# Kernel tuning notes

Hardware: AMD Instinct MI355X
Metric: run time of the kernel (lower is better)

The kernel has to match this reference:

```python
import jax, jax.numpy as jnp
import numpy as np
import jax.ops

N_NODES = 50000
N_EDGES = 800000
N_GRAPHS = 512
F_IN = 128
HID = 256
N_CLASSES = 1

def _xavier(key, shape):
    fan_in, fan_out = shape[0], shape[1]
    std = (2.0 / (fan_in + fan_out)) ** 0.5
    return jax.random.normal(key, shape, dtype=jnp.float32) * std

def setup_inputs() -> dict:
    key = jax.random.key(0)
    ks = jax.random.split(key, 12)
    x = jax.random.normal(ks[0], (N_NODES, F_IN), dtype=jnp.float32)
    edge_index = jax.random.randint(ks[1], (2, N_EDGES), 0, N_NODES, dtype=jnp.int64)
    batch = jnp.sort(jax.random.randint(ks[2], (N_NODES,), 0, N_GRAPHS, dtype=jnp.int64))
    return {
        'x': x, 'edge_index': edge_index, 'batch': batch,
        'W0': _xavier(ks[3], (F_IN, HID)), 'b0': jnp.zeros((HID,), jnp.float32),
        'W1': _xavier(ks[4], (HID, HID)), 'b1': jnp.zeros((HID,), jnp.float32),
        'W2': _xavier(ks[5], (HID, HID)), 'b2': jnp.zeros((HID,), jnp.float32),
        'Wm1': _xavier(ks[6], (HID, HID)), 'bm1': jnp.zeros((HID,), jnp.float32),
        'Wm2': _xavier(ks[7], (HID, N_CLASSES)), 'bm2': jnp.zeros((N_CLASSES,), jnp.float32),
    }

def _gcn_layer(h, W, b, src, dst, deg_inv_sqrt):
    # PyG GCNConv: linear -> symmetric-normalized aggregation (with self loops) -> bias
    hw = h @ W                                        # [N, out]
    norm = deg_inv_sqrt[src] * deg_inv_sqrt[dst]      # [E]
    msg = hw[src] * norm[:, None]                     # [E, out]
    agg = jax.ops.segment_sum(msg, dst, num_segments=N_NODES)
    agg = agg + hw * (deg_inv_sqrt ** 2)[:, None]     # self-loop term
    return agg + b

def reference(x, edge_index, batch, W0, b0, W1, b1, W2, b2, Wm1, bm1, Wm2, bm2):
    src, dst = edge_index[0], edge_index[1]
    # degree with added self loops (in-degree at dst)
    deg = jax.ops.segment_sum(jnp.ones((N_EDGES,), jnp.float32), dst, num_segments=N_NODES) + 1.0
    deg_inv_sqrt = jax.lax.rsqrt(deg)
    h = jax.nn.relu(_gcn_layer(x, W0, b0, src, dst, deg_inv_sqrt))
    h = jax.nn.relu(_gcn_layer(h, W1, b1, src, dst, deg_inv_sqrt))
    h = jax.nn.relu(_gcn_layer(h, W2, b2, src, dst, deg_inv_sqrt))
    # global mean pool over graphs
    sums = jax.ops.segment_sum(h, batch, num_segments=N_GRAPHS)
    cnts = jax.ops.segment_sum(jnp.ones((N_NODES,), jnp.float32), batch, num_segments=N_GRAPHS)
    pooled = sums / jnp.maximum(cnts, 1.0)[:, None]   # [G, HID]
    out = jax.nn.relu(pooled @ Wm1 + bm1) @ Wm2 + bm2 # [G, num_classes]
    return out
```

## Files before the change

kernel.cpp:

```cpp
#include <hip/hip_runtime.h>

constexpr int N_NODES  = 50000;
constexpr int N_EDGES  = 800000;
constexpr int N_GRAPHS = 512;
constexpr int F_IN     = 128;
constexpr int HID      = 256;
constexpr int NPAD     = 50048;

typedef short short8 __attribute__((ext_vector_type(8)));
typedef float f32x4  __attribute__((ext_vector_type(4)));

__device__ __forceinline__ unsigned short f2b(float f) {
    unsigned u = __float_as_uint(f);
    u += 0x7fffu + ((u >> 16) & 1u);
    return (unsigned short)(u >> 16);
}
__device__ __forceinline__ float b2f_lo(unsigned u) { return __uint_as_float(u << 16); }
__device__ __forceinline__ float b2f_hi(unsigned u) { return __uint_as_float(u & 0xffff0000u); }

__global__ __launch_bounds__(256) void prep_kernel(
    const int* __restrict__ dst, int* __restrict__ deg,
    const float* __restrict__ W0, const float* __restrict__ W1, const float* __restrict__ W2,
    unsigned short* __restrict__ Wt0, unsigned short* __restrict__ Wt1, unsigned short* __restrict__ Wt2)
{
    const int b = blockIdx.x, t = threadIdx.x;
    if (b < 3125) {
        int e = b * 256 + t;
        atomicAdd(&deg[dst[e]], 1);
    } else {
        int i = (b - 3125) * 256 + t;
        const float* W; unsigned short* Wt; int K; int j;
        if (i < 32768)      { W = W0; Wt = Wt0; K = 128; j = i; }
        else if (i < 98304) { W = W1; Wt = Wt1; K = 256; j = i - 32768; }
        else                { W = W2; Wt = Wt2; K = 256; j = i - 98304; }
        int k = j >> 8, n = j & 255;
        int idx = (n >> 7) * (K * 128) + (((k >> 3) * 128 + (n & 127)) << 3) + (k & 7);
        Wt[idx] = f2b(W[j]);
    }
}

__global__ void block_sum_dis_kernel(const int* __restrict__ deg, int* __restrict__ bsum,
                                     float* __restrict__ dis, int* __restrict__ bcnt, int n) {
    __shared__ int sm[256];
    __shared__ int hist[64];
    int t = threadIdx.x, base = blockIdx.x * 1024;
    if (t < 64) hist[t] = 0;
    __syncthreads();
    int s = 0;
    #pragma unroll
    for (int i = 0; i < 4; ++i) {
        int idx = base + t + i * 256;
        if (idx < n) {
            int d = deg[idx]; s += d;
            dis[idx] = rsqrtf((float)d + 1.0f);
            atomicAdd(&hist[63 - min(d, 63)], 1);
        }
    }
    sm[t] = s; __syncthreads();
    for (int o = 128; o > 0; o >>= 1) { if (t < o) sm[t] += sm[t + o]; __syncthreads(); }
    if (t == 0) bsum[blockIdx.x] = sm[0];
    if (t < 64 && hist[t]) atomicAdd(&bcnt[t], hist[t]);
}

__global__ void scan_bsum_kernel(int* __restrict__ bsum, int nb,
                                 const int* __restrict__ bcnt, int* __restrict__ bcur) {
    __shared__ int sm[64], sb[64];
    int t = threadIdx.x;
    int v = (t < nb) ? bsum[t] : 0;
    int c = bcnt[t];
    sm[t] = v; sb[t] = c; __syncthreads();
    for (int o = 1; o < 64; o <<= 1) {
        int a = (t >= o) ? sm[t - o] : 0;
        int bb = (t >= o) ? sb[t - o] : 0;
        __syncthreads();
        sm[t] += a; sb[t] += bb;
        __syncthreads();
    }
    if (t < nb) bsum[t] = sm[t] - v;
    bcur[t] = sb[t] - c;
}

__global__ void scan_local_kernel(const int* __restrict__ deg, const int* __restrict__ bsum,
                                  int* __restrict__ cursor, int* __restrict__ bcur,
                                  int4* __restrict__ perm4, int* __restrict__ idx_of,
                                  const float* __restrict__ dis, int n) {
    __shared__ int sm[256];
    __shared__ int lcnt[64], lbase[64];
    int t = threadIdx.x, base = blockIdx.x * 1024;
    if (t < 64) lcnt[t] = 0;
    int idx0 = base + t * 4;
    int v[4], s = 0;
    #pragma unroll
    for (int i = 0; i < 4; ++i) { int id = idx0 + i; v[i] = (id < n) ? deg[id] : 0; s += v[i]; }
    sm[t] = s; __syncthreads();
    for (int o = 1; o < 256; o <<= 1) {
        int a = (t >= o) ? sm[t - o] : 0; __syncthreads();
        sm[t] += a; __syncthreads();
    }
    int excl = bsum[blockIdx.x] + sm[t] - s;
    int st[4], lp[4];
    #pragma unroll
    for (int i = 0; i < 4; ++i) {
        int id = idx0 + i;
        st[i] = excl;
        if (id < n) {
            cursor[id] = excl;
            lp[i] = atomicAdd(&lcnt[63 - min(v[i], 63)], 1);
        }
        excl += v[i];
    }
    __syncthreads();
    if (t < 64) lbase[t] = lcnt[t] ? atomicAdd(&bcur[t], lcnt[t]) : 0;
    __syncthreads();
    #pragma unroll
    for (int i = 0; i < 4; ++i) {
        int id = idx0 + i;
        if (id < n) {
            int hb = 63 - min(v[i], 63);
            int pos = lbase[hb] + lp[i];
            perm4[pos] = make_int4(id, st[i], st[i] + v[i], __float_as_int(dis[id]));
            idx_of[id] = pos;
        }
    }
}

__global__ void fill_csr(const int* __restrict__ src, const int* __restrict__ dst,
                         const float* __restrict__ dis, const int* __restrict__ idx_of,
                         int* __restrict__ cursor, int2* __restrict__ csr) {
    int e = blockIdx.x * blockDim.x + threadIdx.x;
    if (e >= N_EDGES) return;
    int s = src[e], d = dst[e];
    int pos = atomicAdd(&cursor[d], 1);
    float w = dis[s] * dis[d];
    csr[pos] = make_int2(idx_of[s], __float_as_int(w));
}

__global__ __launch_bounds__(256) void xconv_kernel(
    const float* __restrict__ x, const int4* __restrict__ perm4,
    unsigned short* __restrict__ x_bf)
{
    int t = threadIdx.x;
    int idx = blockIdx.x * 64 + (t >> 2);
    if (idx >= N_NODES) return;
    int node = perm4[idx].x;
    int c = t & 3;
    const float4* xs = reinterpret_cast<const float4*>(x + (size_t)node * 128 + c * 32);
    unsigned short* dp = x_bf + (size_t)idx * 128 + c * 32;
    #pragma unroll
    for (int u = 0; u < 8; ++u) {
        float4 v = xs[u];
        unsigned r0 = (unsigned)f2b(v.x) | ((unsigned)f2b(v.y) << 16);
        unsigned r1 = (unsigned)f2b(v.z) | ((unsigned)f2b(v.w) << 16);
        *reinterpret_cast<uint2*>(dp + u * 4) = make_uint2(r0, r1);
    }
}

template<int F>
__global__ __launch_bounds__(256) void agg_full(
    const unsigned short* __restrict__ hin, const int4* __restrict__ perm4,
    const int2* __restrict__ csr, uint4* __restrict__ out4)
{
    constexpr int LPR  = F / 8;
    constexpr int NSUB = 64 / LPR;
    constexpr int EPS  = 16 / NSUB;
    const int lane = threadIdx.x & 63;
    const int sub  = lane / LPR;
    const int fc   = lane % LPR;
    const int idx  = blockIdx.x * 4 + (threadIdx.x >> 6);
    if (idx >= N_NODES) return;
    const int4 p = perm4[idx];
    const float dn = __int_as_float(p.w);

    float acc[8];
    {
        float sw = (sub == 0) ? dn * dn : 0.0f;
        uint2 u2[2];
        *reinterpret_cast<uint4*>(u2) =
            *reinterpret_cast<const uint4*>(hin + (size_t)idx * F + fc * 8);
        #pragma unroll
        for (int h = 0; h < 2; ++h) {
            acc[h * 4 + 0] = b2f_lo(u2[h].x) * sw;
            acc[h * 4 + 1] = b2f_hi(u2[h].x) * sw;
            acc[h * 4 + 2] = b2f_lo(u2[h].y) * sw;
            acc[h * 4 + 3] = b2f_hi(u2[h].y) * sw;
        }
    }

    int j = p.y;
    const int end = p.z;

    for (; j + 16 <= end; j += 16) {
        int2 c[EPS];
        uint2 g[EPS][2];
        #pragma unroll
        for (int u = 0; u < EPS; ++u) c[u] = csr[j + sub * EPS + u];
        #pragma unroll
        for (int u = 0; u < EPS; ++u)
            *reinterpret_cast<uint4*>(g[u]) =
                *reinterpret_cast<const uint4*>(hin + (size_t)c[u].x * F + fc * 8);
        #pragma unroll
        for (int u = 0; u < EPS; ++u) {
            float w = __int_as_float(c[u].y);
            #pragma unroll
            for (int h = 0; h < 2; ++h) {
                acc[h * 4 + 0] = fmaf(b2f_lo(g[u][h].x), w, acc[h * 4 + 0]);
                acc[h * 4 + 1] = fmaf(b2f_hi(g[u][h].x), w, acc[h * 4 + 1]);
                acc[h * 4 + 2] = fmaf(b2f_lo(g[u][h].y), w, acc[h * 4 + 2]);
                acc[h * 4 + 3] = fmaf(b2f_hi(g[u][h].y), w, acc[h * 4 + 3]);
            }
        }
    }
    int jj = j + sub;
    for (; jj + NSUB < end; jj += 2 * NSUB) {
        int2 c0 = csr[jj], c1 = csr[jj + NSUB];
        uint2 g0[2], g1[2];
        *reinterpret_cast<uint4*>(g0) =
            *reinterpret_cast<const uint4*>(hin + (size_t)c0.x * F + fc * 8);
        *reinterpret_cast<uint4*>(g1) =
            *reinterpret_cast<const uint4*>(hin + (size_t)c1.x * F + fc * 8);
        float w0 = __int_as_float(c0.y), w1 = __int_as_float(c1.y);
        #pragma unroll
        for (int h = 0; h < 2; ++h) {
            acc[h * 4 + 0] = fmaf(b2f_lo(g0[h].x), w0, fmaf(b2f_lo(g1[h].x), w1, acc[h * 4 + 0]));
            acc[h * 4 + 1] = fmaf(b2f_hi(g0[h].x), w0, fmaf(b2f_hi(g1[h].x), w1, acc[h * 4 + 1]));
            acc[h * 4 + 2] = fmaf(b2f_lo(g0[h].y), w0, fmaf(b2f_lo(g1[h].y), w1, acc[h * 4 + 2]));
            acc[h * 4 + 3] = fmaf(b2f_hi(g0[h].y), w0, fmaf(b2f_hi(g1[h].y), w1, acc[h * 4 + 3]));
        }
    }
    if (jj < end) {
        int2 c0 = csr[jj];
        float w = __int_as_float(c0.y);
        uint2 g[2];
        *reinterpret_cast<uint4*>(g) =
            *reinterpret_cast<const uint4*>(hin + (size_t)c0.x * F + fc * 8);
        #pragma unroll
        for (int h = 0; h < 2; ++h) {
            acc[h * 4 + 0] = fmaf(b2f_lo(g[h].x), w, acc[h * 4 + 0]);
            acc[h * 4 + 1] = fmaf(b2f_hi(g[h].x), w, acc[h * 4 + 1]);
            acc[h * 4 + 2] = fmaf(b2f_lo(g[h].y), w, acc[h * 4 + 2]);
            acc[h * 4 + 3] = fmaf(b2f_hi(g[h].y), w, acc[h * 4 + 3]);
        }
    }

    #pragma unroll
    for (int k = 0; k < 8; ++k) {
        #pragma unroll
        for (int off = LPR; off < 64; off <<= 1)
            acc[k] += __shfl_xor(acc[k], off, 64);
    }

    if (sub == 0) {
        uint2 r[2];
        #pragma unroll
        for (int h = 0; h < 2; ++h) {
            r[h].x = (unsigned)f2b(acc[h * 4 + 0]) | ((unsigned)f2b(acc[h * 4 + 1]) << 16);
            r[h].y = (unsigned)f2b(acc[h * 4 + 2]) | ((unsigned)f2b(acc[h * 4 + 3]) << 16);
        }
        int chunk = (idx >> 7) * (128 * (F / 8)) + fc * 128 + (idx & 127);
        out4[chunk] = *reinterpret_cast<uint4*>(r);
    }
}

template<int K>
__global__ __launch_bounds__(256) void gemm_frag(
    const uint4* __restrict__ A4,
    const unsigned short* __restrict__ Wt_frag,
    const float* __restrict__ bias,
    unsigned short* __restrict__ C,
    int relu)
{
    __shared__ __align__(16) unsigned short Bs[K * 128];
    const int t    = threadIdx.x;
    const int lane = t & 63;
    const int w    = t >> 6;
    const int wm   = w & 1, wn = w >> 1;
    const int q    = lane >> 4, m = lane & 15;
    const int panel = blockIdx.x;
    const int col0  = blockIdx.y * 128;

    {
        const uint4* src4 = reinterpret_cast<const uint4*>(Wt_frag + blockIdx.y * (K * 128));
        uint4* dst4 = reinterpret_cast<uint4*>(Bs);
        #pragma unroll
        for (int it = 0; it < K / 16; ++it)
            dst4[it * 256 + t] = src4[it * 256 + t];
    }
    __syncthreads();

    f32x4 acc[4][4] = {};
    const int abase = panel * (128 * (K / 8));

    #pragma unroll
    for (int kb = 0; kb < K / 32; ++kb) {
        short8 af[4], bf[4];
        #pragma unroll
        for (int i = 0; i < 4; ++i) {
            uint4 v = A4[abase + (kb * 4 + q) * 128 + wm * 64 + i * 16 + m];
            af[i] = *reinterpret_cast<short8*>(&v);
        }
        #pragma unroll
        for (int jn = 0; jn < 4; ++jn)
            bf[jn] = *reinterpret_cast<const short8*>(&Bs[((kb * 4 + q) * 128 + wn * 64 + jn * 16 + m) * 8]);
        #pragma unroll
        for (int i = 0; i < 4; ++i)
            #pragma unroll
            for (int jn = 0; jn < 4; ++jn)
                acc[i][jn] = __builtin_amdgcn_mfma_f32_16x16x32_bf16(af[i], bf[jn], acc[i][jn], 0, 0, 0);
    }

    #pragma unroll
    for (int jn = 0; jn < 4; ++jn) {
        int col = col0 + wn * 64 + jn * 16 + m;
        float bj = bias[col];
        #pragma unroll
        for (int i = 0; i < 4; ++i) {
            int rowb = panel * 128 + wm * 64 + i * 16 + q * 4;
            #pragma unroll
            for (int r = 0; r < 4; ++r) {
                float v = acc[i][jn][r] + bj;
                if (relu) v = fmaxf(v, 0.f);
                C[(size_t)(rowb + r) * 256 + col] = f2b(v);
            }
        }
    }
}

__global__ __launch_bounds__(256) void pool_mlp_kernel(
    const unsigned short* __restrict__ h, const int* __restrict__ batch,
    const int* __restrict__ idx_of,
    const float* __restrict__ Wm1, const float* __restrict__ bm1,
    const float* __restrict__ Wm2, const float* __restrict__ bm2,
    float* __restrict__ out)
{
    __shared__ float p[HID];
    __shared__ float red[HID];
    __shared__ int se[2];
    const int g = blockIdx.x, t = threadIdx.x;
    if (t < 2) {
        int target = g + t;
        int lo = 0, hi = N_NODES;
        while (lo < hi) { int mid = (lo + hi) >> 1; if (batch[mid] < target) lo = mid + 1; else hi = mid; }
        se[t] = lo;
    }
    __syncthreads();
    const int s = se[0], e = se[1];
    float acc = 0.f;
    int n = s;
    for (; n + 8 <= e; n += 8) {
        int ix[8]; float v[8];
        #pragma unroll
        for (int u = 0; u < 8; ++u) ix[u] = idx_of[n + u];
        #pragma unroll
        for (int u = 0; u < 8; ++u) v[u] = b2f_lo((unsigned)h[(size_t)ix[u] * HID + t]);
        acc += ((v[0] + v[1]) + (v[2] + v[3])) + ((v[4] + v[5]) + (v[6] + v[7]));
    }
    for (; n < e; ++n)
        acc += b2f_lo((unsigned)h[(size_t)idx_of[n] * HID + t]);
    p[t] = acc / fmaxf((float)(e - s), 1.0f);
    __syncthreads();
    float a2 = bm1[t];
    for (int k = 0; k < HID; ++k) a2 = fmaf(p[k], Wm1[k * HID + t], a2);
    red[t] = fmaxf(a2, 0.f) * Wm2[t];
    __syncthreads();
    for (int o = 128; o > 0; o >>= 1) {
        if (t < o) red[t] += red[t + o];
        __syncthreads();
    }
    if (t == 0) out[g] = red[0] + bm2[0];
}

extern "C" void kernel_launch(void* const* d_in, const int* in_sizes, int n_in,
                              void* d_out, int out_size, void* d_ws, size_t ws_size,
                              hipStream_t stream) {
    const float* x    = (const float*)d_in[0];
    const int*   ei   = (const int*)d_in[1];
    const int*   batch= (const int*)d_in[2];
    const float* W0   = (const float*)d_in[3];
    const float* b0   = (const float*)d_in[4];
    const float* W1   = (const float*)d_in[5];
    const float* b1   = (const float*)d_in[6];
    const float* W2   = (const float*)d_in[7];
    const float* b2   = (const float*)d_in[8];
    const float* Wm1  = (const float*)d_in[9];
    const float* bm1  = (const float*)d_in[10];
    const float* Wm2  = (const float*)d_in[11];
    const float* bm2  = (const float*)d_in[12];
    float* out = (float*)d_out;

    char* ws = (char*)d_ws;
    size_t off = 0;
    auto alloc = [&](size_t bytes) -> void* {
        void* p = ws + off;
        off += (bytes + 255) & ~(size_t)255;
        return p;
    };
    int*   deg    = (int*)  alloc((size_t)N_NODES * 4);
    int*   bcnt   = (int*)  alloc(64 * 4);
    int*   bcur   = (int*)  alloc(64 * 4);
    float* dis    = (float*)alloc((size_t)N_NODES * 4);
    int*   cursor = (int*)  alloc((size_t)N_NODES * 4);
    int*   bsum   = (int*)  alloc((size_t)64 * 4);
    int4*  perm4  = (int4*) alloc((size_t)NPAD * 16);
    int*   idx_of = (int*)  alloc((size_t)N_NODES * 4);
    int2*  csr    = (int2*) alloc((size_t)N_EDGES * 8);
    unsigned short* x_bf  = (unsigned short*)alloc((size_t)NPAD * F_IN * 2);
    unsigned short* Wt0   = (unsigned short*)alloc((size_t)F_IN * HID * 2);
    unsigned short* Wt1   = (unsigned short*)alloc((size_t)HID * HID * 2);
    unsigned short* Wt2   = (unsigned short*)alloc((size_t)HID * HID * 2);
    unsigned short* bufA  = (unsigned short*)alloc((size_t)NPAD * HID * 2);
    unsigned short* bufB  = (unsigned short*)alloc((size_t)NPAD * HID * 2);

    const int* src = ei;
    const int* dst = ei + N_EDGES;
    const int NB = (N_NODES + 1023) / 1024;

    size_t zlen = (size_t)((char*)bcur - (char*)deg) + 64 * 4;
    hipMemsetAsync(deg, 0, zlen, stream);

    prep_kernel         <<<3765, 256, 0, stream>>>(dst, deg, W0, W1, W2, Wt0, Wt1, Wt2);
    block_sum_dis_kernel<<<NB, 256, 0, stream>>>(deg, bsum, dis, bcnt, N_NODES);
    scan_bsum_kernel    <<<1, 64, 0, stream>>>(bsum, NB, bcnt, bcur);
    scan_local_kernel   <<<NB, 256, 0, stream>>>(deg, bsum, cursor, bcur, perm4, idx_of, dis, N_NODES);
    fill_csr            <<<(N_EDGES + 255) / 256, 256, 0, stream>>>(src, dst, dis, idx_of, cursor, csr);
    xconv_kernel        <<<NPAD / 64, 256, 0, stream>>>(x, perm4, x_bf);

    dim3 ggrid(NPAD / 128, 2);
    const int AGG_B = (N_NODES + 3) / 4;

    agg_full<F_IN><<<AGG_B, 256, 0, stream>>>(x_bf, perm4, csr, (uint4*)bufA);
    gemm_frag<F_IN><<<ggrid, 256, 0, stream>>>((const uint4*)bufA, Wt0, b0, bufB, 1);

    agg_full<HID><<<AGG_B, 256, 0, stream>>>(bufB, perm4, csr, (uint4*)bufA);
    gemm_frag<HID><<<ggrid, 256, 0, stream>>>((const uint4*)bufA, Wt1, b1, bufB, 1);

    agg_full<HID><<<AGG_B, 256, 0, stream>>>(bufB, perm4, csr, (uint4*)bufA);
    gemm_frag<HID><<<ggrid, 256, 0, stream>>>((const uint4*)bufA, Wt2, b2, bufB, 1);

    pool_mlp_kernel<<<N_GRAPHS, HID, 0, stream>>>(bufB, batch, idx_of, Wm1, bm1, Wm2, bm2, out);
}
```

Measured before the change: 413.2 us.

## Split 256-wide hidden features into two 128-column halves for aggregation

The GEMM now writes its output in a column-split layout, two planes of NPAD x 128. The 256-wide aggregation runs as two half-width blocks per node group, each gathering 256-byte rows from a single plane. The intent is to shrink the working set each gather touches, for better L2/MALL locality, and to double the parallelism with more sub-groups per edge. Pool reads are adjusted to the new layout. The cost is that CSR indices and weights are read twice and the GEMM stores are more scattered.

```diff
diff --git a/kernel.cpp b/kernel.cpp
--- a/kernel.cpp
+++ b/kernel.cpp
@@ -155,14 +155,14 @@
     }
 }
 
-template<int F>
-__global__ __launch_bounds__(256) void agg_full(
+__global__ __launch_bounds__(256) void agg_full128(
     const unsigned short* __restrict__ hin, const int4* __restrict__ perm4,
     const int2* __restrict__ csr, uint4* __restrict__ out4)
 {
-    constexpr int LPR  = F / 8;
-    constexpr int NSUB = 64 / LPR;
-    constexpr int EPS  = 16 / NSUB;
+    constexpr int F    = 128;
+    constexpr int LPR  = 16;
+    constexpr int NSUB = 4;
+    constexpr int EPS  = 4;
     const int lane = threadIdx.x & 63;
     const int sub  = lane / LPR;
     const int fc   = lane % LPR;
@@ -188,7 +188,6 @@
 
     int j = p.y;
     const int end = p.z;
-
     for (; j + 16 <= end; j += 16) {
         int2 c[EPS];
         uint2 g[EPS][2];
@@ -257,6 +256,116 @@
             r[h].y = (unsigned)f2b(acc[h * 4 + 2]) | ((unsigned)f2b(acc[h * 4 + 3]) << 16);
         }
         int chunk = (idx >> 7) * (128 * (F / 8)) + fc * 128 + (idx & 127);
+        out4[chunk] = *reinterpret_cast<uint4*>(r);
+    }
+}
+
+__global__ __launch_bounds__(256) void agg_split256(
+    const unsigned short* __restrict__ hin, const int4* __restrict__ perm4,
+    const int2* __restrict__ csr, uint4* __restrict__ out4)
+{
+    constexpr int ROW  = 128;
+    constexpr int LPR  = 16;
+    constexpr int NSUB = 4;
+    constexpr int EPS  = 4;
+    const int gid  = blockIdx.x;
+    const int hh   = gid & 1;
+    const int nb   = gid >> 1;
+    const int lane = threadIdx.x & 63;
+    const int sub  = lane / LPR;
+    const int fcl  = lane % LPR;
+    const int idx  = nb * 4 + (threadIdx.x >> 6);
+    if (idx >= N_NODES) return;
+    const int4 p = perm4[idx];
+    const float dn = __int_as_float(p.w);
+    const unsigned short* hb = hin + (size_t)hh * NPAD * ROW;
+
+    float acc[8];
+    {
+        float sw = (sub == 0) ? dn * dn : 0.0f;
+        uint2 u2[2];
+        *reinterpret_cast<uint4*>(u2) =
+            *reinterpret_cast<const uint4*>(hb + (size_t)idx * ROW + fcl * 8);
+        #pragma unroll
+        for (int h = 0; h < 2; ++h) {
+            acc[h * 4 + 0] = b2f_lo(u2[h].x) * sw;
+            acc[h * 4 + 1] = b2f_hi(u2[h].x) * sw;
+            acc[h * 4 + 2] = b2f_lo(u2[h].y) * sw;
+            acc[h * 4 + 3] = b2f_hi(u2[h].y) * sw;
+        }
+    }
+
+    int j = p.y;
+    const int end = p.z;
+    for (; j + 16 <= end; j += 16) {
+        int2 c[EPS];
+        uint2 g[EPS][2];
+        #pragma unroll
+        for (int u = 0; u < EPS; ++u) c[u] = csr[j + sub * EPS + u];
+        #pragma unroll
+        for (int u = 0; u < EPS; ++u)
+            *reinterpret_cast<uint4*>(g[u]) =
+                *reinterpret_cast<const uint4*>(hb + (size_t)c[u].x * ROW + fcl * 8);
+        #pragma unroll
+        for (int u = 0; u < EPS; ++u) {
+            float w = __int_as_float(c[u].y);
+            #pragma unroll
+            for (int h = 0; h < 2; ++h) {
+                acc[h * 4 + 0] = fmaf(b2f_lo(g[u][h].x), w, acc[h * 4 + 0]);
+                acc[h * 4 + 1] = fmaf(b2f_hi(g[u][h].x), w, acc[h * 4 + 1]);
+                acc[h * 4 + 2] = fmaf(b2f_lo(g[u][h].y), w, acc[h * 4 + 2]);
+                acc[h * 4 + 3] = fmaf(b2f_hi(g[u][h].y), w, acc[h * 4 + 3]);
+            }
+        }
+    }
+    int jj = j + sub;
+    for (; jj + NSUB < end; jj += 2 * NSUB) {
+        int2 c0 = csr[jj], c1 = csr[jj + NSUB];
+        uint2 g0[2], g1[2];
+        *reinterpret_cast<uint4*>(g0) =
+            *reinterpret_cast<const uint4*>(hb + (size_t)c0.x * ROW + fcl * 8);
+        *reinterpret_cast<uint4*>(g1) =
+            *reinterpret_cast<const uint4*>(hb + (size_t)c1.x * ROW + fcl * 8);
+        float w0 = __int_as_float(c0.y), w1 = __int_as_float(c1.y);
+        #pragma unroll
+        for (int h = 0; h < 2; ++h) {
+            acc[h * 4 + 0] = fmaf(b2f_lo(g0[h].x), w0, fmaf(b2f_lo(g1[h].x), w1, acc[h * 4 + 0]));
+            acc[h * 4 + 1] = fmaf(b2f_hi(g0[h].x), w0, fmaf(b2f_hi(g1[h].x), w1, acc[h * 4 + 1]));
+            acc[h * 4 + 2] = fmaf(b2f_lo(g0[h].y), w0, fmaf(b2f_lo(g1[h].y), w1, acc[h * 4 + 2]));
+            acc[h * 4 + 3] = fmaf(b2f_hi(g0[h].y), w0, fmaf(b2f_hi(g1[h].y), w1, acc[h * 4 + 3]));
+        }
+    }
+    if (jj < end) {
+        int2 c0 = csr[jj];
+        float w = __int_as_float(c0.y);
+        uint2 g[2];
+        *reinterpret_cast<uint4*>(g) =
+            *reinterpret_cast<const uint4*>(hb + (size_t)c0.x * ROW + fcl * 8);
+        #pragma unroll
+        for (int h = 0; h < 2; ++h) {
+            acc[h * 4 + 0] = fmaf(b2f_lo(g[h].x), w, acc[h * 4 + 0]);
+            acc[h * 4 + 1] = fmaf(b2f_hi(g[h].x), w, acc[h * 4 + 1]);
+            acc[h * 4 + 2] = fmaf(b2f_lo(g[h].y), w, acc[h * 4 + 2]);
+            acc[h * 4 + 3] = fmaf(b2f_hi(g[h].y), w, acc[h * 4 + 3]);
+        }
+    }
+
+    #pragma unroll
+    for (int k = 0; k < 8; ++k) {
+        #pragma unroll
+        for (int off = LPR; off < 64; off <<= 1)
+            acc[k] += __shfl_xor(acc[k], off, 64);
+    }
+
+    if (sub == 0) {
+        uint2 r[2];
+        #pragma unroll
+        for (int h = 0; h < 2; ++h) {
+            r[h].x = (unsigned)f2b(acc[h * 4 + 0]) | ((unsigned)f2b(acc[h * 4 + 1]) << 16);
+            r[h].y = (unsigned)f2b(acc[h * 4 + 2]) | ((unsigned)f2b(acc[h * 4 + 3]) << 16);
+        }
+        int fc = hh * LPR + fcl;
+        int chunk = (idx >> 7) * (128 * 32) + fc * 128 + (idx & 127);
         out4[chunk] = *reinterpret_cast<uint4*>(r);
     }
 }
@@ -312,6 +421,7 @@
     for (int jn = 0; jn < 4; ++jn) {
         int col = col0 + wn * 64 + jn * 16 + m;
         float bj = bias[col];
+        int ch = col >> 7, cc = col & 127;
         #pragma unroll
         for (int i = 0; i < 4; ++i) {
             int rowb = panel * 128 + wm * 64 + i * 16 + q * 4;
@@ -319,7 +429,7 @@
             for (int r = 0; r < 4; ++r) {
                 float v = acc[i][jn][r] + bj;
                 if (relu) v = fmaxf(v, 0.f);
-                C[(size_t)(rowb + r) * 256 + col] = f2b(v);
+                C[((size_t)ch * NPAD + (rowb + r)) * 128 + cc] = f2b(v);
             }
         }
     }
@@ -344,6 +454,7 @@
     }
     __syncthreads();
     const int s = se[0], e = se[1];
+    const size_t cbase = (size_t)(t >> 7) * ((size_t)NPAD * 128) + (t & 127);
     float acc = 0.f;
     int n = s;
     for (; n + 8 <= e; n += 8) {
@@ -351,11 +462,11 @@
         #pragma unroll
         for (int u = 0; u < 8; ++u) ix[u] = idx_of[n + u];
         #pragma unroll
-        for (int u = 0; u < 8; ++u) v[u] = b2f_lo((unsigned)h[(size_t)ix[u] * HID + t]);
+        for (int u = 0; u < 8; ++u) v[u] = b2f_lo((unsigned)h[cbase + (size_t)ix[u] * 128]);
         acc += ((v[0] + v[1]) + (v[2] + v[3])) + ((v[4] + v[5]) + (v[6] + v[7]));
     }
     for (; n < e; ++n)
-        acc += b2f_lo((unsigned)h[(size_t)idx_of[n] * HID + t]);
+        acc += b2f_lo((unsigned)h[cbase + (size_t)idx_of[n] * 128]);
     p[t] = acc / fmaxf((float)(e - s), 1.0f);
     __syncthreads();
     float a2 = bm1[t];
@@ -427,13 +538,13 @@
     dim3 ggrid(NPAD / 128, 2);
     const int AGG_B = (N_NODES + 3) / 4;
 
-    agg_full<F_IN><<<AGG_B, 256, 0, stream>>>(x_bf, perm4, csr, (uint4*)bufA);
+    agg_full128<<<AGG_B, 256, 0, stream>>>(x_bf, perm4, csr, (uint4*)bufA);
     gemm_frag<F_IN><<<ggrid, 256, 0, stream>>>((const uint4*)bufA, Wt0, b0, bufB, 1);
 
-    agg_full<HID><<<AGG_B, 256, 0, stream>>>(bufB, perm4, csr, (uint4*)bufA);
+    agg_split256<<<AGG_B * 2, 256, 0, stream>>>(bufB, perm4, csr, (uint4*)bufA);
     gemm_frag<HID><<<ggrid, 256, 0, stream>>>((const uint4*)bufA, Wt1, b1, bufB, 1);
 
-    agg_full<HID><<<AGG_B, 256, 0, stream>>>(bufB, perm4, csr, (uint4*)bufA);
+    agg_split256<<<AGG_B * 2, 256, 0, stream>>>(bufB, perm4, csr, (uint4*)bufA);
     gemm_frag<HID><<<ggrid, 256, 0, stream>>>((const uint4*)bufA, Wt2, b2, bufB, 1);
 
     pool_mlp_kernel<<<N_GRAPHS, HID, 0, stream>>>(bufB, batch, idx_of, Wm1, bm1, Wm2, bm2, out);
```

Result: no change. 407.9 us (-1.3%).

## Split feature rows into two column halves for aggregation and fuse CSR fill with conversion

Applied to the files above, without the earlier changes.

Node feature buffers are stored as two column-half planes (each NPAD x F/2), and aggregation launches twice as many blocks, each gathering only one half. Each gather then touches a half-size working set, which should improve cache hit rates for the random neighbour reads. The GEMM epilogue, the x conversion and pooling are updated to write and read the split layout. The CSR fill and x conversion kernels are merged into one launch, and the CSR reads and output stores use nontemporal hints. The cost is that the edge list is read twice per layer and the indexing is more complex.

```diff
diff --git a/kernel.cpp b/kernel.cpp
--- a/kernel.cpp
+++ b/kernel.cpp
@@ -9,6 +9,8 @@
 
 typedef short short8 __attribute__((ext_vector_type(8)));
 typedef float f32x4  __attribute__((ext_vector_type(4)));
+typedef unsigned int u32x4 __attribute__((ext_vector_type(4)));
+typedef unsigned int u32x2 __attribute__((ext_vector_type(2)));
 
 __device__ __forceinline__ unsigned short f2b(float f) {
     unsigned u = __float_as_uint(f);
@@ -124,59 +126,64 @@
     }
 }
 
-__global__ void fill_csr(const int* __restrict__ src, const int* __restrict__ dst,
-                         const float* __restrict__ dis, const int* __restrict__ idx_of,
-                         int* __restrict__ cursor, int2* __restrict__ csr) {
-    int e = blockIdx.x * blockDim.x + threadIdx.x;
-    if (e >= N_EDGES) return;
-    int s = src[e], d = dst[e];
-    int pos = atomicAdd(&cursor[d], 1);
-    float w = dis[s] * dis[d];
-    csr[pos] = make_int2(idx_of[s], __float_as_int(w));
-}
-
-__global__ __launch_bounds__(256) void xconv_kernel(
+__global__ __launch_bounds__(256) void fillcsr_xconv_kernel(
+    const int* __restrict__ src, const int* __restrict__ dst,
+    const float* __restrict__ dis, const int* __restrict__ idx_of,
+    int* __restrict__ cursor, int2* __restrict__ csr,
     const float* __restrict__ x, const int4* __restrict__ perm4,
     unsigned short* __restrict__ x_bf)
 {
-    int t = threadIdx.x;
-    int idx = blockIdx.x * 64 + (t >> 2);
-    if (idx >= N_NODES) return;
-    int node = perm4[idx].x;
-    int c = t & 3;
-    const float4* xs = reinterpret_cast<const float4*>(x + (size_t)node * 128 + c * 32);
-    unsigned short* dp = x_bf + (size_t)idx * 128 + c * 32;
-    #pragma unroll
-    for (int u = 0; u < 8; ++u) {
-        float4 v = xs[u];
-        unsigned r0 = (unsigned)f2b(v.x) | ((unsigned)f2b(v.y) << 16);
-        unsigned r1 = (unsigned)f2b(v.z) | ((unsigned)f2b(v.w) << 16);
-        *reinterpret_cast<uint2*>(dp + u * 4) = make_uint2(r0, r1);
+    const int b = blockIdx.x, t = threadIdx.x;
+    if (b < 3125) {
+        int e = b * 256 + t;
+        int s = src[e], d = dst[e];
+        int pos = atomicAdd(&cursor[d], 1);
+        float w = dis[s] * dis[d];
+        csr[pos] = make_int2(idx_of[s], __float_as_int(w));
+    } else {
+        int idx = (b - 3125) * 64 + (t >> 2);
+        if (idx >= N_NODES) return;
+        int node = perm4[idx].x;
+        int c = t & 3;
+        const float4* xs = reinterpret_cast<const float4*>(x + (size_t)node * 128 + c * 32);
+        unsigned short* dp = x_bf + ((size_t)(c >> 1) * NPAD + idx) * 64 + (c & 1) * 32;
+        #pragma unroll
+        for (int u = 0; u < 8; ++u) {
+            float4 v = xs[u];
+            unsigned r0 = (unsigned)f2b(v.x) | ((unsigned)f2b(v.y) << 16);
+            unsigned r1 = (unsigned)f2b(v.z) | ((unsigned)f2b(v.w) << 16);
+            *reinterpret_cast<uint2*>(dp + u * 4) = make_uint2(r0, r1);
+        }
     }
 }
 
 template<int F>
-__global__ __launch_bounds__(256) void agg_full(
+__global__ __launch_bounds__(256) void agg_split(
     const unsigned short* __restrict__ hin, const int4* __restrict__ perm4,
     const int2* __restrict__ csr, uint4* __restrict__ out4)
 {
-    constexpr int LPR  = F / 8;
+    constexpr int ROW  = F / 2;
+    constexpr int LPR  = ROW / 8;
     constexpr int NSUB = 64 / LPR;
     constexpr int EPS  = 16 / NSUB;
+    const int gid  = blockIdx.x;
+    const int hh   = gid & 1;
+    const int nb   = gid >> 1;
     const int lane = threadIdx.x & 63;
     const int sub  = lane / LPR;
-    const int fc   = lane % LPR;
-    const int idx  = blockIdx.x * 4 + (threadIdx.x >> 6);
+    const int fcl  = lane % LPR;
+    const int idx  = nb * 4 + (threadIdx.x >> 6);
     if (idx >= N_NODES) return;
     const int4 p = perm4[idx];
     const float dn = __int_as_float(p.w);
+    const unsigned short* hb = hin + (size_t)hh * NPAD * ROW;
 
     float acc[8];
     {
         float sw = (sub == 0) ? dn * dn : 0.0f;
         uint2 u2[2];
         *reinterpret_cast<uint4*>(u2) =
-            *reinterpret_cast<const uint4*>(hin + (size_t)idx * F + fc * 8);
+            *reinterpret_cast<const uint4*>(hb + (size_t)idx * ROW + fcl * 8);
         #pragma unroll
         for (int h = 0; h < 2; ++h) {
             acc[h * 4 + 0] = b2f_lo(u2[h].x) * sw;
@@ -188,19 +195,20 @@
 
     int j = p.y;
     const int end = p.z;
-
     for (; j + 16 <= end; j += 16) {
-        int2 c[EPS];
+        u32x2 c[EPS];
         uint2 g[EPS][2];
         #pragma unroll
-        for (int u = 0; u < EPS; ++u) c[u] = csr[j + sub * EPS + u];
+        for (int u = 0; u < EPS; ++u)
+            c[u] = __builtin_nontemporal_load(
+                reinterpret_cast<const u32x2*>(&csr[j + sub * EPS + u]));
         #pragma unroll
         for (int u = 0; u < EPS; ++u)
             *reinterpret_cast<uint4*>(g[u]) =
-                *reinterpret_cast<const uint4*>(hin + (size_t)c[u].x * F + fc * 8);
+                *reinterpret_cast<const uint4*>(hb + (size_t)(int)c[u].x * ROW + fcl * 8);
         #pragma unroll
         for (int u = 0; u < EPS; ++u) {
-            float w = __int_as_float(c[u].y);
+            float w = __uint_as_float(c[u].y);
             #pragma unroll
             for (int h = 0; h < 2; ++h) {
                 acc[h * 4 + 0] = fmaf(b2f_lo(g[u][h].x), w, acc[h * 4 + 0]);
@@ -212,13 +220,14 @@
     }
     int jj = j + sub;
     for (; jj + NSUB < end; jj += 2 * NSUB) {
-        int2 c0 = csr[jj], c1 = csr[jj + NSUB];
+        u32x2 c0 = __builtin_nontemporal_load(reinterpret_cast<const u32x2*>(&csr[jj]));
+        u32x2 c1 = __builtin_nontemporal_load(reinterpret_cast<const u32x2*>(&csr[jj + NSUB]));
         uint2 g0[2], g1[2];
         *reinterpret_cast<uint4*>(g0) =
-            *reinterpret_cast<const uint4*>(hin + (size_t)c0.x * F + fc * 8);
+            *reinterpret_cast<const uint4*>(hb + (size_t)(int)c0.x * ROW + fcl * 8);
         *reinterpret_cast<uint4*>(g1) =
-            *reinterpret_cast<const uint4*>(hin + (size_t)c1.x * F + fc * 8);
-        float w0 = __int_as_float(c0.y), w1 = __int_as_float(c1.y);
+            *reinterpret_cast<const uint4*>(hb + (size_t)(int)c1.x * ROW + fcl * 8);
+        float w0 = __uint_as_float(c0.y), w1 = __uint_as_float(c1.y);
         #pragma unroll
         for (int h = 0; h < 2; ++h) {
             acc[h * 4 + 0] = fmaf(b2f_lo(g0[h].x), w0, fmaf(b2f_lo(g1[h].x), w1, acc[h * 4 + 0]));
@@ -228,11 +237,11 @@
         }
     }
     if (jj < end) {
-        int2 c0 = csr[jj];
-        float w = __int_as_float(c0.y);
+        u32x2 c0 = __builtin_nontemporal_load(reinterpret_cast<const u32x2*>(&csr[jj]));
+        float w = __uint_as_float(c0.y);
         uint2 g[2];
         *reinterpret_cast<uint4*>(g) =
-            *reinterpret_cast<const uint4*>(hin + (size_t)c0.x * F + fc * 8);
+            *reinterpret_cast<const uint4*>(hb + (size_t)(int)c0.x * ROW + fcl * 8);
         #pragma unroll
         for (int h = 0; h < 2; ++h) {
             acc[h * 4 + 0] = fmaf(b2f_lo(g[h].x), w, acc[h * 4 + 0]);
@@ -250,14 +259,14 @@
     }
 
     if (sub == 0) {
-        uint2 r[2];
-        #pragma unroll
-        for (int h = 0; h < 2; ++h) {
-            r[h].x = (unsigned)f2b(acc[h * 4 + 0]) | ((unsigned)f2b(acc[h * 4 + 1]) << 16);
-            r[h].y = (unsigned)f2b(acc[h * 4 + 2]) | ((unsigned)f2b(acc[h * 4 + 3]) << 16);
-        }
+        u32x4 r;
+        r.x = (unsigned)f2b(acc[0]) | ((unsigned)f2b(acc[1]) << 16);
+        r.y = (unsigned)f2b(acc[2]) | ((unsigned)f2b(acc[3]) << 16);
+        r.z = (unsigned)f2b(acc[4]) | ((unsigned)f2b(acc[5]) << 16);
+        r.w = (unsigned)f2b(acc[6]) | ((unsigned)f2b(acc[7]) << 16);
+        int fc = hh * LPR + fcl;
         int chunk = (idx >> 7) * (128 * (F / 8)) + fc * 128 + (idx & 127);
-        out4[chunk] = *reinterpret_cast<uint4*>(r);
+        __builtin_nontemporal_store(r, reinterpret_cast<u32x4*>(&out4[chunk]));
     }
 }
 
@@ -312,6 +321,7 @@
     for (int jn = 0; jn < 4; ++jn) {
         int col = col0 + wn * 64 + jn * 16 + m;
         float bj = bias[col];
+        int ch = col >> 7, cc = col & 127;
         #pragma unroll
         for (int i = 0; i < 4; ++i) {
             int rowb = panel * 128 + wm * 64 + i * 16 + q * 4;
@@ -319,7 +329,7 @@
             for (int r = 0; r < 4; ++r) {
                 float v = acc[i][jn][r] + bj;
                 if (relu) v = fmaxf(v, 0.f);
-                C[(size_t)(rowb + r) * 256 + col] = f2b(v);
+                C[((size_t)ch * NPAD + (rowb + r)) * 128 + cc] = f2b(v);
             }
         }
     }
@@ -344,6 +354,7 @@
     }
     __syncthreads();
     const int s = se[0], e = se[1];
+    const size_t cbase = (size_t)(t >> 7) * ((size_t)NPAD * 128) + (t & 127);
     float acc = 0.f;
     int n = s;
     for (; n + 8 <= e; n += 8) {
@@ -351,11 +362,12 @@
         #pragma unroll
         for (int u = 0; u < 8; ++u) ix[u] = idx_of[n + u];
         #pragma unroll
-        for (int u = 0; u < 8; ++u) v[u] = b2f_lo((unsigned)h[(size_t)ix[u] * HID + t]);
+        for (int u = 0; u < 8; ++u)
+            v[u] = b2f_lo((unsigned)__builtin_nontemporal_load(&h[cbase + (size_t)ix[u] * 128]));
         acc += ((v[0] + v[1]) + (v[2] + v[3])) + ((v[4] + v[5]) + (v[6] + v[7]));
     }
     for (; n < e; ++n)
-        acc += b2f_lo((unsigned)h[(size_t)idx_of[n] * HID + t]);
+        acc += b2f_lo((unsigned)__builtin_nontemporal_load(&h[cbase + (size_t)idx_of[n] * 128]));
     p[t] = acc / fmaxf((float)(e - s), 1.0f);
     __syncthreads();
     float a2 = bm1[t];
@@ -421,19 +433,19 @@
     block_sum_dis_kernel<<<NB, 256, 0, stream>>>(deg, bsum, dis, bcnt, N_NODES);
     scan_bsum_kernel    <<<1, 64, 0, stream>>>(bsum, NB, bcnt, bcur);
     scan_local_kernel   <<<NB, 256, 0, stream>>>(deg, bsum, cursor, bcur, perm4, idx_of, dis, N_NODES);
-    fill_csr            <<<(N_EDGES + 255) / 256, 256, 0, stream>>>(src, dst, dis, idx_of, cursor, csr);
-    xconv_kernel        <<<NPAD / 64, 256, 0, stream>>>(x, perm4, x_bf);
+    fillcsr_xconv_kernel<<<3125 + 782, 256, 0, stream>>>(src, dst, dis, idx_of, cursor, csr,
+                                                         x, perm4, x_bf);
 
     dim3 ggrid(NPAD / 128, 2);
     const int AGG_B = (N_NODES + 3) / 4;
 
-    agg_full<F_IN><<<AGG_B, 256, 0, stream>>>(x_bf, perm4, csr, (uint4*)bufA);
+    agg_split<F_IN><<<AGG_B * 2, 256, 0, stream>>>(x_bf, perm4, csr, (uint4*)bufA);
     gemm_frag<F_IN><<<ggrid, 256, 0, stream>>>((const uint4*)bufA, Wt0, b0, bufB, 1);
 
-    agg_full<HID><<<AGG_B, 256, 0, stream>>>(bufB, perm4, csr, (uint4*)bufA);
+    agg_split<HID><<<AGG_B * 2, 256, 0, stream>>>(bufB, perm4, csr, (uint4*)bufA);
     gemm_frag<HID><<<ggrid, 256, 0, stream>>>((const uint4*)bufA, Wt1, b1, bufB, 1);
 
-    agg_full<HID><<<AGG_B, 256, 0, stream>>>(bufB, perm4, csr, (uint4*)bufA);
+    agg_split<HID><<<AGG_B * 2, 256, 0, stream>>>(bufB, perm4, csr, (uint4*)bufA);
     gemm_frag<HID><<<ggrid, 256, 0, stream>>>((const uint4*)bufA, Wt2, b2, bufB, 1);
 
     pool_mlp_kernel<<<N_GRAPHS, HID, 0, stream>>>(bufB, batch, idx_of, Wm1, bm1, Wm2, bm2, out);
```

Result: slower. 445.4 us (+7.8%).
